# Kernel optimization log

Measured on AMD Instinct MI355X. Metric: run time of the kernel, lower is better.

Reference implementation:

```python
import jax, jax.numpy as jnp
import numpy as np

L, N, E, H, R = 2048, 4, 768, 12, 16
ALPHA = 16.0
LORA_SCALE = ALPHA / R
HEAD_DIM = E // H


def setup_inputs() -> dict:
    rng = jax.random.key(0)
    ks = jax.random.split(rng, 15)
    g = lambda i, shape, s=1.0: jax.random.normal(ks[i], shape, jnp.float32) * s
    return {
        "query": g(0, (L, N, E)),
        "key": g(1, (L, N, E)),
        "value": g(2, (L, N, E)),
        "in_proj_weight": g(3, (3 * E, E), 0.02),
        "in_proj_bias": g(4, (3 * E,), 0.02),
        "q_down": g(5, (R, E), 0.02),
        "q_up": g(6, (E, R), 0.02),
        "k_down": g(7, (R, E), 0.02),
        "k_up": g(8, (E, R), 0.02),
        "v_down": g(9, (R, E), 0.02),
        "v_up": g(10, (E, R), 0.02),
        "out_proj_weight": g(11, (E, E), 0.02),
        "out_proj_bias": g(12, (E,), 0.02),
        "out_down": g(13, (R, E), 0.02),
        "out_up": g(14, (E, R), 0.02),
    }


def _lora_linear(x, W, b, down, up):
    # y = x W^T + b + scale * (x down^T) up^T   (LoRA-adapted nn.Linear)
    return x @ W.T + b + LORA_SCALE * ((x @ down.T) @ up.T)


def reference(query, key, value, in_proj_weight, in_proj_bias,
              q_down, q_up, k_down, k_up, v_down, v_up,
              out_proj_weight, out_proj_bias, out_down, out_up):
    Wq, Wk, Wv = jnp.split(in_proj_weight, 3, axis=0)
    bq, bk, bv = jnp.split(in_proj_bias, 3)
    q = _lora_linear(query, Wq, bq, q_down, q_up)   # (L,N,E)
    k = _lora_linear(key, Wk, bk, k_down, k_up)     # (S,N,E)
    v = _lora_linear(value, Wv, bv, v_down, v_up)

    def to_heads(t):  # (T,N,E) -> (N,H,T,hd)
        return t.reshape(t.shape[0], N, H, HEAD_DIM).transpose(1, 2, 0, 3)

    qh, kh, vh = to_heads(q), to_heads(k), to_heads(v)
    scale = 1.0 / jnp.sqrt(jnp.float32(HEAD_DIM))
    scores = jnp.einsum('nhld,nhsd->nhls', qh * scale, kh)  # (N,H,L,S)
    attn = jax.nn.softmax(scores, axis=-1)
    o = jnp.einsum('nhls,nhsd->nhld', attn, vh)             # (N,H,L,hd)
    o = o.transpose(2, 0, 1, 3).reshape(L, N, E)            # (L,N,E)
    return _lora_linear(o, out_proj_weight, out_proj_bias, out_down, out_up)
```

## Files before the change

### kernel.cpp

```cpp
#include <hip/hip_runtime.h>

#define LL 2048
#define NN 4
#define EE 768
#define HH 12
#define RR 16
#define HD 64
#define TT (LL*NN)
#define F3 (3*EE)

typedef __bf16 bf16;
typedef bf16 bf16x4 __attribute__((ext_vector_type(4)));
typedef bf16 bf16x8 __attribute__((ext_vector_type(8)));
typedef float floatx4 __attribute__((ext_vector_type(4)));
typedef float floatx16 __attribute__((ext_vector_type(16)));
typedef unsigned uintx4 __attribute__((ext_vector_type(4)));

#define ZERO16 (floatx16){0.f,0.f,0.f,0.f,0.f,0.f,0.f,0.f,0.f,0.f,0.f,0.f,0.f,0.f,0.f,0.f}

__device__ __forceinline__ unsigned pk_bf16(float a, float b) {
    unsigned r;
    asm("v_cvt_pk_bf16_f32 %0, %1, %2" : "=v"(r) : "v"(a), "v"(b));
    return r;
}

__global__ __launch_bounds__(256) void prep_w(
    const float* __restrict__ W,  const float* __restrict__ qu,
    const float* __restrict__ ku, const float* __restrict__ vu,
    const float* __restrict__ Wo, const float* __restrict__ ou,
    const float* __restrict__ qd, const float* __restrict__ kd,
    const float* __restrict__ vd, const float* __restrict__ odw,
    bf16* __restrict__ Wa)
{
    const int f0 = blockIdx.x * 16;
    const int tid = threadIdx.x;

    const float* Wsrc;
    const float* up;
    const float* dn;
    if (f0 < F3) {
        const int third = f0 / EE, fe = f0 % EE;
        Wsrc = W + (size_t)f0*EE;
        up   = ((third == 0) ? qu : (third == 1) ? ku : vu) + (size_t)fe*RR;
        dn   = (third == 0) ? qd : (third == 1) ? kd : vd;
    } else {
        const int fe = f0 - F3;
        Wsrc = Wo + (size_t)fe*EE;
        up   = ou + (size_t)fe*RR;
        dn   = odw;
    }

    float dnv[3][RR];
    #pragma unroll
    for (int i = 0; i < 3; ++i)
        #pragma unroll
        for (int r = 0; r < RR; ++r)
            dnv[i][r] = dn[(size_t)r*EE + i*256 + tid];

    for (int fr = 0; fr < 16; ++fr) {
        float u[RR];
        #pragma unroll
        for (int r = 0; r < RR; ++r) u[r] = up[(size_t)fr*RR + r];
        bf16* orow = Wa + (size_t)(f0 + fr)*EE;
        #pragma unroll
        for (int i = 0; i < 3; ++i) {
            float acc = Wsrc[(size_t)fr*EE + i*256 + tid];
            #pragma unroll
            for (int r = 0; r < RR; ++r) acc += u[r] * dnv[i][r];
            orow[i*256 + tid] = (bf16)acc;
        }
    }
}

template<int MODE>
__global__ __launch_bounds__(256, 2) void gemm_aug(
    const float* __restrict__ Aq, const float* __restrict__ Ak,
    const float* __restrict__ Av, const bf16* __restrict__ Abf,
    const bf16* __restrict__ B,
    const float* __restrict__ bias,
    bf16* __restrict__ qo, bf16* __restrict__ ko, bf16* __restrict__ vo,
    float* __restrict__ fo)
{
    __shared__ bf16 AsA[128][64], BsA[128][64];
    __shared__ bf16 AsB[128][64], BsB[128][64];
    const int t0 = blockIdx.x * 128;
    const int f0 = blockIdx.y * 128;
    const int tid = threadIdx.x;
    const int wave = tid >> 6, lane = tid & 63;
    const int quad = lane >> 4, l16 = lane & 15;
    const int m0 = (wave & 1) * 64;
    const int n0 = (wave >> 1) * 64;
    const int swr = l16 & 7;

    const int third = (MODE == 0) ? (f0 / EE) : 0;
    const float* A32 = (MODE == 0)
        ? ((third == 0) ? Aq : (third == 1) ? Ak : Av) : nullptr;

    const int r0 = tid >> 3, cg = tid & 7;
    const int gsw = cg ^ (r0 & 7);

    float4 ga0[4], ga1[4];
    bf16x8 gab[4];
    bf16x8 gbb[4];

#define LOADT(kb) do {                                                        \
        _Pragma("unroll")                                                     \
        for (int c = 0; c < 4; ++c) {                                         \
            if constexpr (MODE == 0) {                                        \
                const float* src =                                            \
                    A32 + (size_t)(t0 + c*32 + r0)*EE + (kb)*64 + cg*8;       \
                ga0[c] = *(const float4*)(src);                               \
                ga1[c] = *(const float4*)(src + 4);                           \
            } else {                                                          \
                gab[c] = *(const bf16x8*)(                                    \
                    Abf + (size_t)(t0 + c*32 + r0)*EE + (kb)*64 + cg*8);      \
            }                                                                 \
            gbb[c] = *(const bf16x8*)(                                        \
                B + (size_t)(f0 + c*32 + r0)*EE + (kb)*64 + cg*8);            \
        }                                                                     \
    } while (0)
#define STORET(AS, BS) do {                                                   \
        _Pragma("unroll")                                                     \
        for (int c = 0; c < 4; ++c) {                                         \
            if constexpr (MODE == 0) {                                        \
                union { uintx4 u; bf16x8 h; } cv;                             \
                cv.u = (uintx4){ pk_bf16(ga0[c].x, ga0[c].y),                 \
                                 pk_bf16(ga0[c].z, ga0[c].w),                 \
                                 pk_bf16(ga1[c].x, ga1[c].y),                 \
                                 pk_bf16(ga1[c].z, ga1[c].w) };               \
                *(bf16x8*)(&AS[c*32 + r0][gsw*8]) = cv.h;                     \
            } else {                                                          \
                *(bf16x8*)(&AS[c*32 + r0][gsw*8]) = gab[c];                   \
            }                                                                 \
            *(bf16x8*)(&BS[c*32 + r0][gsw*8]) = gbb[c];                       \
        }                                                                     \
    } while (0)
#define COMPUTE(AS, BS) do {                                                  \
        _Pragma("unroll")                                                     \
        for (int kc = 0; kc < 2; ++kc) {                                      \
            bf16x8 a[4], bfr[4];                                              \
            _Pragma("unroll")                                                 \
            for (int rt = 0; rt < 4; ++rt)                                    \
                a[rt] = *(const bf16x8*)(                                     \
                    &AS[m0 + rt*16 + l16][((kc*4 + quad) ^ swr) * 8]);        \
            _Pragma("unroll")                                                 \
            for (int ct = 0; ct < 4; ++ct)                                    \
                bfr[ct] = *(const bf16x8*)(                                   \
                    &BS[n0 + ct*16 + l16][((kc*4 + quad) ^ swr) * 8]);        \
            _Pragma("unroll")                                                 \
            for (int rt = 0; rt < 4; ++rt)                                    \
                _Pragma("unroll")                                             \
                for (int ct = 0; ct < 4; ++ct)                                \
                    acc[rt][ct] = __builtin_amdgcn_mfma_f32_16x16x32_bf16(    \
                        a[rt], bfr[ct], acc[rt][ct], 0, 0, 0);                \
        }                                                                     \
    } while (0)

    floatx4 acc[4][4];
    #pragma unroll
    for (int rt = 0; rt < 4; ++rt)
        #pragma unroll
        for (int ct = 0; ct < 4; ++ct) acc[rt][ct] = (floatx4){0.f,0.f,0.f,0.f};

    const int NT = EE/64;
    LOADT(0);
    STORET(AsA, BsA);
    LOADT(1);
    __syncthreads();

    for (int tt = 0; tt < NT/2; ++tt) {
        STORET(AsB, BsB);
        { int k2 = 2*tt + 2; if (k2 >= NT) k2 -= NT; LOADT(k2); }
        COMPUTE(AsA, BsA);
        __syncthreads();
        STORET(AsA, BsA);
        { int k3 = 2*tt + 3; if (k3 >= NT) k3 -= NT; LOADT(k3); }
        COMPUTE(AsB, BsB);
        __syncthreads();
    }
#undef LOADT
#undef STORET
#undef COMPUTE

    #pragma unroll
    for (int rt = 0; rt < 4; ++rt) {
        #pragma unroll
        for (int r = 0; r < 4; ++r) {
            const int t = t0 + m0 + rt*16 + quad*4 + r;
            #pragma unroll
            for (int ct = 0; ct < 4; ++ct) {
                const int fl = n0 + ct*16 + l16;
                float c = acc[rt][ct][r] + bias[f0 + fl];
                if (MODE == 0) {
                    const int fe = (f0 % EE) + fl;
                    const int h = fe >> 6, d = fe & 63;
                    const int l = t >> 2, n = t & 3;
                    const size_t idx = (((size_t)(n*HH + h)*LL) + l)*HD + d;
                    if (third == 0)      qo[idx] = (bf16)(c * 0.180336877f);
                    else if (third == 1) ko[idx] = (bf16)c;
                    else                 vo[idx] = (bf16)c;
                } else {
                    fo[(size_t)t*EE + f0 + fl] = c;
                }
            }
        }
    }
}

__global__ __launch_bounds__(256) void vtrans(
    const bf16* __restrict__ vin, bf16* __restrict__ vout)
{
    __shared__ bf16 T[64][64];
    const int nh = blockIdx.x >> 5;
    const int l0 = (blockIdx.x & 31) * 64;
    const int tid = threadIdx.x;
    const bf16* src = vin + ((size_t)nh*LL + l0)*HD;
    #pragma unroll
    for (int c = 0; c < 2; ++c) {
        int id = c*256 + tid;
        int row = id >> 3, dg = id & 7;
        int pg = dg ^ (row & 7);
        *(bf16x8*)(&T[row][pg*8]) = *(const bf16x8*)(src + row*HD + dg*8);
    }
    __syncthreads();
    bf16* dst = vout + (size_t)nh*HD*LL;
    const int wave = tid >> 6, lane = tid & 63;
    #pragma unroll
    for (int it = 0; it < 2; ++it) {
        const int d  = it*32 + wave*8 + (lane >> 3);
        const int cg = lane & 7;
        bf16x8 vv;
        #pragma unroll
        for (int j = 0; j < 8; ++j) {
            const int lrow = cg*8 + j;
            const int pg = (d >> 3) ^ (lrow & 7);
            vv[j] = T[lrow][pg*8 + (d & 7)];
        }
        *(bf16x8*)(dst + (size_t)d*LL + l0 + cg*8) = vv;
    }
}

__device__ __forceinline__ void compute_tile(
    const bf16 (&KS)[64][64], const bf16 (&VS)[64][64],
    const bf16x8 (&bq)[4], const bf16x8& ones, const floatx16& z16,
    int l32, int hi, int sw,
    floatx16& oacc0, floatx16& oacc1, floatx16& oaccS)
{
    #pragma unroll
    for (int ss = 0; ss < 2; ++ss) {
        bf16x8 ak[4];
        #pragma unroll
        for (int t4 = 0; t4 < 4; ++t4)
            ak[t4] = *(const bf16x8*)(&KS[ss*32 + l32][((t4*2 + hi) ^ sw) * 8]);

        __builtin_amdgcn_s_setprio(1);
        floatx16 sacc = __builtin_amdgcn_mfma_f32_32x32x16_bf16(
            ak[0], bq[0], z16, 0, 0, 0);
        #pragma unroll
        for (int t4 = 1; t4 < 4; ++t4)
            sacc = __builtin_amdgcn_mfma_f32_32x32x16_bf16(
                ak[t4], bq[t4], sacc, 0, 0, 0);
        __builtin_amdgcn_s_setprio(0);

        bf16x8 bv[4];
        #pragma unroll
        for (int tl = 0; tl < 2; ++tl)
            #pragma unroll
            for (int dt = 0; dt < 2; ++dt)
                bv[tl*2 + dt] = *(const bf16x8*)(
                    &VS[dt*32 + l32][((ss*4 + tl*2 + hi) ^ sw) * 8]);

        float p[16];
        #pragma unroll
        for (int r = 0; r < 16; ++r) p[r] = __builtin_amdgcn_exp2f(sacc[r]);

        union { uintx4 u; bf16x8 h; } fr0, fr1;
        {
            unsigned c0 = pk_bf16(p[0], p[1]);
            unsigned c1 = pk_bf16(p[2], p[3]);
            unsigned c2 = pk_bf16(p[4], p[5]);
            unsigned c3 = pk_bf16(p[6], p[7]);
            asm("v_permlane32_swap_b32 %0, %1" : "+v"(c0), "+v"(c2));
            asm("v_permlane32_swap_b32 %0, %1" : "+v"(c1), "+v"(c3));
            fr0.u = (uintx4){c0, c1, c2, c3};
        }
        {
            unsigned c0 = pk_bf16(p[8],  p[9]);
            unsigned c1 = pk_bf16(p[10], p[11]);
            unsigned c2 = pk_bf16(p[12], p[13]);
            unsigned c3 = pk_bf16(p[14], p[15]);
            asm("v_permlane32_swap_b32 %0, %1" : "+v"(c0), "+v"(c2));
            asm("v_permlane32_swap_b32 %0, %1" : "+v"(c1), "+v"(c3));
            fr1.u = (uintx4){c0, c1, c2, c3};
        }

        __builtin_amdgcn_s_setprio(1);
        oaccS = __builtin_amdgcn_mfma_f32_32x32x16_bf16(fr0.h, ones, oaccS, 0, 0, 0);
        oaccS = __builtin_amdgcn_mfma_f32_32x32x16_bf16(fr1.h, ones, oaccS, 0, 0, 0);
        oacc0 = __builtin_amdgcn_mfma_f32_32x32x16_bf16(fr0.h, bv[0], oacc0, 0, 0, 0);
        oacc1 = __builtin_amdgcn_mfma_f32_32x32x16_bf16(fr0.h, bv[1], oacc1, 0, 0, 0);
        oacc0 = __builtin_amdgcn_mfma_f32_32x32x16_bf16(fr1.h, bv[2], oacc0, 0, 0, 0);
        oacc1 = __builtin_amdgcn_mfma_f32_32x32x16_bf16(fr1.h, bv[3], oacc1, 0, 0, 0);
        __builtin_amdgcn_s_setprio(0);
    }
}

__global__ __launch_bounds__(256, 3) void attn_mfma(
    const bf16* __restrict__ qf, const bf16* __restrict__ kf,
    const bf16* __restrict__ vf, bf16* __restrict__ Oa)
{
    __shared__ bf16 KsA[64][64], VtA[64][64];
    __shared__ bf16 KsB[64][64], VtB[64][64];

    const int bid = blockIdx.x;
    const int nh = bid % 48;
    const int l0 = (bid / 48) * 128;
    const int tid  = threadIdx.x;
    const int wave = tid >> 6;
    const int lane = tid & 63;
    const int l32  = lane & 31;
    const int hi   = lane >> 5;
    const int sw   = l32 & 7;

    const bf16* qb = qf + (size_t)nh * LL * HD;
    const bf16* kb = kf + (size_t)nh * LL * HD;
    const bf16* vb = vf + (size_t)nh * HD * LL;

    const int q0 = l0 + wave * 32;

    const int rowA = tid >> 3;
    const int rowB = rowA + 32;
    const int g0   = tid & 7;
    const int gsA  = g0 ^ (rowA & 7);

    const bf16* pK0 = kb + (size_t)rowA*HD + g0*8;
    const bf16* pK1 = kb + (size_t)rowB*HD + g0*8;
    const bf16* pV0 = vb + (size_t)rowA*LL + g0*8;
    const bf16* pV1 = vb + (size_t)rowB*LL + g0*8;

    bf16x8 bq[4];
    #pragma unroll
    for (int t = 0; t < 4; ++t)
        bq[t] = *(const bf16x8*)(qb + (size_t)(q0 + l32)*HD + t*16 + hi*8);

    const bf16x8 ones = { (bf16)1.f, (bf16)1.f, (bf16)1.f, (bf16)1.f,
                          (bf16)1.f, (bf16)1.f, (bf16)1.f, (bf16)1.f };
    const floatx16 z16 = ZERO16;

    floatx16 oacc0 = ZERO16;
    floatx16 oacc1 = ZERO16;
    floatx16 oaccS = ZERO16;

    bf16x8 gk0, gk1, gv0, gv1;

#define LOADT(S) do {                                                         \
        gk0 = *(const bf16x8*)(pK0 + (size_t)(S)*HD);                         \
        gk1 = *(const bf16x8*)(pK1 + (size_t)(S)*HD);                         \
        gv0 = *(const bf16x8*)(pV0 + (S));                                    \
        gv1 = *(const bf16x8*)(pV1 + (S));                                    \
    } while (0)
#define STORE_A() do {                                                        \
        *(bf16x8*)(&KsA[rowA][gsA*8]) = gk0;                                  \
        *(bf16x8*)(&KsA[rowB][gsA*8]) = gk1;                                  \
        *(bf16x8*)(&VtA[rowA][gsA*8]) = gv0;                                  \
        *(bf16x8*)(&VtA[rowB][gsA*8]) = gv1;                                  \
    } while (0)
#define STORE_B() do {                                                        \
        *(bf16x8*)(&KsB[rowA][gsA*8]) = gk0;                                  \
        *(bf16x8*)(&KsB[rowB][gsA*8]) = gk1;                                  \
        *(bf16x8*)(&VtB[rowA][gsA*8]) = gv0;                                  \
        *(bf16x8*)(&VtB[rowB][gsA*8]) = gv1;                                  \
    } while (0)

    LOADT(0);
    STORE_A();
    LOADT(64);
    __syncthreads();

    for (int tt = 0; tt < 16; ++tt) {
        STORE_B();
        LOADT((size_t)((2*tt + 2) & 31) * 64);
        compute_tile(KsA, VtA, bq, ones, z16, l32, hi, sw, oacc0, oacc1, oaccS);
        __syncthreads();
        STORE_A();
        LOADT((size_t)((2*tt + 3) & 31) * 64);
        compute_tile(KsB, VtB, bq, ones, z16, l32, hi, sw, oacc0, oacc1, oaccS);
        __syncthreads();
    }
#undef LOADT
#undef STORE_A
#undef STORE_B

    const int n = nh / HH, h = nh % HH;
    #pragma unroll
    for (int r = 0; r < 16; ++r) {
        const int qloc = (r & 3) + 8*(r >> 2) + 4*hi;
        const float iv = 1.f / oaccS[r];
        const size_t t = (size_t)(q0 + qloc)*NN + n;
        Oa[t*EE + h*64 + l32]      = (bf16)(oacc0[r] * iv);
        Oa[t*EE + h*64 + 32 + l32] = (bf16)(oacc1[r] * iv);
    }
}

extern "C" void kernel_launch(void* const* d_in, const int* in_sizes, int n_in,
                              void* d_out, int out_size, void* d_ws, size_t ws_size,
                              hipStream_t stream) {
    const float* q   = (const float*)d_in[0];
    const float* k   = (const float*)d_in[1];
    const float* v   = (const float*)d_in[2];
    const float* W   = (const float*)d_in[3];
    const float* b   = (const float*)d_in[4];
    const float* qd  = (const float*)d_in[5];
    const float* qu  = (const float*)d_in[6];
    const float* kd  = (const float*)d_in[7];
    const float* ku  = (const float*)d_in[8];
    const float* vd  = (const float*)d_in[9];
    const float* vu  = (const float*)d_in[10];
    const float* Wo  = (const float*)d_in[11];
    const float* bo  = (const float*)d_in[12];
    const float* odw = (const float*)d_in[13];
    const float* ou  = (const float*)d_in[14];
    float* out = (float*)d_out;

    char* wsb = (char*)d_ws;
    bf16* vfb = (bf16*)wsb;
    bf16* Oa  = (bf16*)(wsb + (size_t)TT*EE*2);
    bf16* Wa  = (bf16*)(wsb + (size_t)3*TT*EE*2);
    bf16* qfb = Wa + (size_t)3072*EE;
    bf16* kfb = qfb + (size_t)TT*EE;
    bf16* vld = kfb + (size_t)TT*EE;

    prep_w<<<192, 256, 0, stream>>>(W, qu, ku, vu, Wo, ou, qd, kd, vd, odw, Wa);
    gemm_aug<0><<<dim3(TT/128, F3/128), 256, 0, stream>>>(
        q, k, v, nullptr, Wa, b, qfb, kfb, vld, nullptr);
    vtrans<<<48*32, 256, 0, stream>>>(vld, vfb);
    attn_mfma<<<48*16, 256, 0, stream>>>(qfb, kfb, vfb, Oa);
    gemm_aug<1><<<dim3(TT/128, EE/128), 256, 0, stream>>>(
        nullptr, nullptr, nullptr, Oa, Wa + (size_t)F3*EE, bo,
        nullptr, nullptr, nullptr, out);
}
```

Before: 277.0 us.

## Use single-buffered 128-wide K tiles in projection GEMM instead of double-buffered 64

The projection GEMM now stages 128-wide K slices in a single LDS buffer per operand, replacing the two 64-wide ping-pong buffers. This halves the number of K iterations and lets each barrier cover more MFMA work, with the XOR swizzle widened to 16 chunks. In exchange, each thread holds twice as many prefetch registers (16 float4 for fp32 A), and the LDS store now sits between two barriers instead of overlapping compute. That adds serialization and register pressure and may reduce occupancy under launch_bounds(256,2).

```diff
diff --git a/kernel.cpp b/kernel.cpp
--- a/kernel.cpp
+++ b/kernel.cpp
@@ -81,8 +81,8 @@
     bf16* __restrict__ qo, bf16* __restrict__ ko, bf16* __restrict__ vo,
     float* __restrict__ fo)
 {
-    __shared__ bf16 AsA[128][64], BsA[128][64];
-    __shared__ bf16 AsB[128][64], BsB[128][64];
+    __shared__ bf16 As[128][128];
+    __shared__ bf16 Bs[128][128];
     const int t0 = blockIdx.x * 128;
     const int f0 = blockIdx.y * 128;
     const int tid = threadIdx.x;
@@ -90,63 +90,65 @@
     const int quad = lane >> 4, l16 = lane & 15;
     const int m0 = (wave & 1) * 64;
     const int n0 = (wave >> 1) * 64;
-    const int swr = l16 & 7;
 
     const int third = (MODE == 0) ? (f0 / EE) : 0;
     const float* A32 = (MODE == 0)
         ? ((third == 0) ? Aq : (third == 1) ? Ak : Av) : nullptr;
 
-    const int r0 = tid >> 3, cg = tid & 7;
-    const int gsw = cg ^ (r0 & 7);
-
-    float4 ga0[4], ga1[4];
-    bf16x8 gab[4];
-    bf16x8 gbb[4];
+    const int sr = tid >> 4;
+    const int sc = tid & 15;
+    const int scp = sc ^ sr;
+
+    float4 ga[16];
+    bf16x8 gab[8];
+    bf16x8 gbb[8];
 
 #define LOADT(kb) do {                                                        \
         _Pragma("unroll")                                                     \
-        for (int c = 0; c < 4; ++c) {                                         \
+        for (int c = 0; c < 8; ++c) {                                         \
+            const int row = c*16 + sr;                                        \
             if constexpr (MODE == 0) {                                        \
                 const float* src =                                            \
-                    A32 + (size_t)(t0 + c*32 + r0)*EE + (kb)*64 + cg*8;       \
-                ga0[c] = *(const float4*)(src);                               \
-                ga1[c] = *(const float4*)(src + 4);                           \
+                    A32 + (size_t)(t0 + row)*EE + (kb)*128 + sc*8;            \
+                ga[2*c]   = *(const float4*)(src);                            \
+                ga[2*c+1] = *(const float4*)(src + 4);                        \
             } else {                                                          \
                 gab[c] = *(const bf16x8*)(                                    \
-                    Abf + (size_t)(t0 + c*32 + r0)*EE + (kb)*64 + cg*8);      \
+                    Abf + (size_t)(t0 + row)*EE + (kb)*128 + sc*8);           \
             }                                                                 \
             gbb[c] = *(const bf16x8*)(                                        \
-                B + (size_t)(f0 + c*32 + r0)*EE + (kb)*64 + cg*8);            \
+                B + (size_t)(f0 + row)*EE + (kb)*128 + sc*8);                 \
         }                                                                     \
     } while (0)
-#define STORET(AS, BS) do {                                                   \
+#define STORET() do {                                                         \
         _Pragma("unroll")                                                     \
-        for (int c = 0; c < 4; ++c) {                                         \
+        for (int c = 0; c < 8; ++c) {                                         \
+            const int row = c*16 + sr;                                        \
             if constexpr (MODE == 0) {                                        \
                 union { uintx4 u; bf16x8 h; } cv;                             \
-                cv.u = (uintx4){ pk_bf16(ga0[c].x, ga0[c].y),                 \
-                                 pk_bf16(ga0[c].z, ga0[c].w),                 \
-                                 pk_bf16(ga1[c].x, ga1[c].y),                 \
-                                 pk_bf16(ga1[c].z, ga1[c].w) };               \
-                *(bf16x8*)(&AS[c*32 + r0][gsw*8]) = cv.h;                     \
+                cv.u = (uintx4){ pk_bf16(ga[2*c].x,   ga[2*c].y),             \
+                                 pk_bf16(ga[2*c].z,   ga[2*c].w),             \
+                                 pk_bf16(ga[2*c+1].x, ga[2*c+1].y),           \
+                                 pk_bf16(ga[2*c+1].z, ga[2*c+1].w) };         \
+                *(bf16x8*)(&As[row][scp*8]) = cv.h;                           \
             } else {                                                          \
-                *(bf16x8*)(&AS[c*32 + r0][gsw*8]) = gab[c];                   \
+                *(bf16x8*)(&As[row][scp*8]) = gab[c];                         \
             }                                                                 \
-            *(bf16x8*)(&BS[c*32 + r0][gsw*8]) = gbb[c];                       \
+            *(bf16x8*)(&Bs[row][scp*8]) = gbb[c];                             \
         }                                                                     \
     } while (0)
-#define COMPUTE(AS, BS) do {                                                  \
+#define COMPUTE() do {                                                        \
         _Pragma("unroll")                                                     \
-        for (int kc = 0; kc < 2; ++kc) {                                      \
+        for (int kc = 0; kc < 4; ++kc) {                                      \
             bf16x8 a[4], bfr[4];                                              \
             _Pragma("unroll")                                                 \
             for (int rt = 0; rt < 4; ++rt)                                    \
                 a[rt] = *(const bf16x8*)(                                     \
-                    &AS[m0 + rt*16 + l16][((kc*4 + quad) ^ swr) * 8]);        \
+                    &As[m0 + rt*16 + l16][((kc*4 + quad) ^ l16) * 8]);        \
             _Pragma("unroll")                                                 \
             for (int ct = 0; ct < 4; ++ct)                                    \
                 bfr[ct] = *(const bf16x8*)(                                   \
-                    &BS[n0 + ct*16 + l16][((kc*4 + quad) ^ swr) * 8]);        \
+                    &Bs[n0 + ct*16 + l16][((kc*4 + quad) ^ l16) * 8]);        \
             _Pragma("unroll")                                                 \
             for (int rt = 0; rt < 4; ++rt)                                    \
                 _Pragma("unroll")                                             \
@@ -162,21 +164,20 @@
         #pragma unroll
         for (int ct = 0; ct < 4; ++ct) acc[rt][ct] = (floatx4){0.f,0.f,0.f,0.f};
 
-    const int NT = EE/64;
+    const int NT = EE/128;
     LOADT(0);
-    STORET(AsA, BsA);
+    STORET();
     LOADT(1);
     __syncthreads();
 
-    for (int tt = 0; tt < NT/2; ++tt) {
-        STORET(AsB, BsB);
-        { int k2 = 2*tt + 2; if (k2 >= NT) k2 -= NT; LOADT(k2); }
-        COMPUTE(AsA, BsA);
+    for (int kb = 0; kb < NT; ++kb) {
+        COMPUTE();
         __syncthreads();
-        STORET(AsA, BsA);
-        { int k3 = 2*tt + 3; if (k3 >= NT) k3 -= NT; LOADT(k3); }
-        COMPUTE(AsB, BsB);
-        __syncthreads();
+        if (kb + 1 < NT) {
+            STORET();
+            if (kb + 2 < NT) LOADT(kb + 2);
+            __syncthreads();
+        }
     }
 #undef LOADT
 #undef STORET
```

After: 274.7 us. About the same (-0.8%).
